# Performance work log

Measured on AMD Instinct MI355X. Metric: run time of the kernel, lower is better.

The kernel has to match this reference:

```python
import jax, jax.numpy as jnp
import numpy as np

N_NODES = 100000
N_EDGES = 1600000
D_IN = 128
D_OUT = 128
NUM_NEIGHBORS = 10


def setup_inputs() -> dict:
    key = jax.random.key(0)
    k1, k2, k3, k4 = jax.random.split(key, 4)
    x = jax.random.normal(k1, (N_NODES, D_IN), dtype=jnp.float32)
    edge_index = jax.random.randint(k2, (2, N_EDGES), 0, N_NODES, dtype=jnp.int64)
    W = jax.random.normal(k3, (D_OUT, D_IN), dtype=jnp.float32) / np.sqrt(D_IN)
    b = jax.random.normal(k4, (D_OUT,), dtype=jnp.float32) * 0.01
    return {"x": x, "edge_index": edge_index, "W": W, "b": b}


def reference(x, edge_index, W, b):
    # Torch semantics: for each node, take the FIRST num_neighbors edges
    # (in original edge order) with row==node, mean their col features;
    # fall back to x[node] if the node has no out-edges. Then linear.
    row, col = edge_index[0], edge_index[1]
    N, E = x.shape[0], row.shape[0]
    # Stable sort by row preserves within-row edge order, so "first k per row"
    # is identical to the torch masking loop.
    order = jnp.argsort(row, stable=True)
    row_s = row[order]
    col_s = col[order]
    # Index of first edge of each row segment -> per-edge rank within segment.
    starts = jnp.searchsorted(row_s, jnp.arange(N, dtype=row_s.dtype))
    rank = jnp.arange(E) - starts[row_s]
    keep = (rank < NUM_NEIGHBORS).astype(x.dtype)  # [E]
    # Masked gather + segment sum == sampled neighbor mean numerator.
    feats = x[col_s] * keep[:, None]               # [E, D_IN] (gather-bound)
    sums = jax.ops.segment_sum(feats, row_s, num_segments=N)
    counts = jax.ops.segment_sum(keep, row_s, num_segments=N)  # [N]
    agg = jnp.where(counts[:, None] > 0,
                    sums / jnp.maximum(counts, 1.0)[:, None],
                    x)
    return agg @ W.T + b
```

## Files before the change

### kernel.cpp

```cpp
#include <hip/hip_runtime.h>
#include <hip/hip_bf16.h>
#include <cstdint>
#include <cstddef>

#define D 128
#define KNB 10
#define SENT 0x7FFFFFFF
#define SHIFT 8
#define NPB 256
#define T_BIN 256
#define EPB 4096
#define MAXNB 1024

typedef __attribute__((ext_vector_type(8))) short short8;
typedef __attribute__((ext_vector_type(4))) float floatx4;

__device__ inline unsigned bf16_rne(float f) {
  unsigned u = __builtin_bit_cast(unsigned, f);
  return (u + 0x7FFFu + ((u >> 16) & 1u)) >> 16;
}
__device__ inline float bflo(unsigned u) { return __builtin_bit_cast(float, u << 16); }
__device__ inline float bfhi(unsigned u) { return __builtin_bit_cast(float, u & 0xFFFF0000u); }

__global__ __launch_bounds__(256) void k_init(int* __restrict__ counts, int NB) {
  int i = blockIdx.x * 256 + threadIdx.x;
  if (i < NB) counts[i] = 0;
}

__global__ __launch_bounds__(T_BIN) void k_count_xcast(const int* __restrict__ row, int E,
                                                       int NB, int* __restrict__ counts,
                                                       int blocks_bin,
                                                       const float* __restrict__ x,
                                                       unsigned* __restrict__ xh, int n8) {
  if ((int)blockIdx.x < blocks_bin) {
    __shared__ int hist[MAXNB];
    for (int i = threadIdx.x; i < NB; i += T_BIN) hist[i] = 0;
    __syncthreads();
    int e0 = blockIdx.x * EPB;
    for (int i = threadIdx.x; i < EPB; i += T_BIN) {
      int e = e0 + i;
      if (e < E) atomicAdd(&hist[row[e] >> SHIFT], 1);
    }
    __syncthreads();
    for (int i = threadIdx.x; i < NB; i += T_BIN)
      if (hist[i]) atomicAdd(&counts[i], hist[i]);
  } else {
    int t = ((int)blockIdx.x - blocks_bin) * T_BIN + threadIdx.x;
    if (t >= n8) return;
    const float4* p = reinterpret_cast<const float4*>(x) + (size_t)t * 2;
    float4 a = p[0], b = p[1];
    uint4 o;
    o.x = bf16_rne(a.x) | (bf16_rne(a.y) << 16);
    o.y = bf16_rne(a.z) | (bf16_rne(a.w) << 16);
    o.z = bf16_rne(b.x) | (bf16_rne(b.y) << 16);
    o.w = bf16_rne(b.z) | (bf16_rne(b.w) << 16);
    reinterpret_cast<uint4*>(xh)[t] = o;
  }
}

__global__ __launch_bounds__(MAXNB) void k_scan(const int* __restrict__ counts, int NB,
                                                int* __restrict__ bases,
                                                int* __restrict__ cursor) {
  __shared__ int buf[MAXNB];
  int t = threadIdx.x;
  int v = (t < NB) ? counts[t] : 0;
  buf[t] = v;
  __syncthreads();
  for (int off = 1; off < MAXNB; off <<= 1) {
    int xv = (t >= off) ? buf[t - off] : 0;
    __syncthreads();
    buf[t] += xv;
    __syncthreads();
  }
  if (t < NB) {
    int base = buf[t] - v;
    bases[t] = base;
    cursor[t] = base;
  }
}

__global__ __launch_bounds__(T_BIN) void k_scatter2(const int* __restrict__ row, int E,
                                                    int NB, int* __restrict__ cursor,
                                                    unsigned* __restrict__ binned) {
  __shared__ int hist[MAXNB];
  __shared__ int lbase[MAXNB];
  for (int i = threadIdx.x; i < NB; i += T_BIN) hist[i] = 0;
  __syncthreads();
  int e0 = blockIdx.x * EPB;
  for (int i = threadIdx.x; i < EPB; i += T_BIN) {
    int e = e0 + i;
    if (e < E) atomicAdd(&hist[row[e] >> SHIFT], 1);
  }
  __syncthreads();
  for (int i = threadIdx.x; i < NB; i += T_BIN) {
    int h = hist[i];
    lbase[i] = h ? atomicAdd(&cursor[i], h) : 0;
  }
  __syncthreads();
  for (int i = threadIdx.x; i < NB; i += T_BIN) hist[i] = 0;
  __syncthreads();
  for (int i = threadIdx.x; i < EPB; i += T_BIN) {
    int e = e0 + i;
    if (e < E) {
      int r = row[e];
      int b = r >> SHIFT;
      int pos = lbase[b] + atomicAdd(&hist[b], 1);
      binned[pos] = ((unsigned)(r & (NPB - 1)) << 24) | (unsigned)e;
    }
  }
}

__global__ __launch_bounds__(256) void k_select(const unsigned* __restrict__ binned,
                                                const int* __restrict__ bases,
                                                const int* __restrict__ counts,
                                                const int* __restrict__ ei,
                                                int* __restrict__ slots_g, int N, int E) {
  __shared__ int sl[NPB * KNB];
  int b = blockIdx.x;
  int nbase = b << SHIFT;
  int nloc = min(NPB, N - nbase);
  for (int i = threadIdx.x; i < nloc * KNB; i += 256) sl[i] = SENT;
  __syncthreads();
  int base = bases[b];
  int cnt = counts[b];
  if (cnt > E) cnt = E;
  for (int i = threadIdx.x; i < cnt; i += 256) {
    unsigned en = binned[base + i];
    int rl = (int)(en >> 24);
    int v = (int)(en & 0xFFFFFFu);
    int* s = &sl[rl * KNB];
#pragma unroll
    for (int k = 0; k < KNB; ++k) {
      int old = atomicMin(&s[k], v);
      if (old == SENT) break;
      v = v > old ? v : old;
    }
  }
  __syncthreads();
  for (int i = threadIdx.x; i < nloc * KNB; i += 256) {
    int v = sl[i];
    int col = ((unsigned)v < (unsigned)E) ? ei[(size_t)E + v] : -1;
    slots_g[(size_t)nbase * KNB + i] = col;
  }
}

__global__ __launch_bounds__(256) void k_agg_hb(const unsigned* __restrict__ xh,
                                                const float* __restrict__ x,
                                                const int* __restrict__ slots,
                                                unsigned* __restrict__ aggbh,
                                                int N) {
  const int lane = threadIdx.x & 63;
  const int j16 = lane & 15;
  const int gsh = lane & 48;
  const int n = blockIdx.x * 16 + (threadIdx.x >> 4);
  const bool active = n < N;

  int scol = -1;
  if (active && j16 < KNB) scol = slots[(size_t)n * KNB + j16];
  bool valid = (unsigned)scol < (unsigned)N;
  unsigned long long bal = __ballot(valid);
  int nsel = __popc((unsigned)((bal >> gsh) & 0xFFFFull));

  int ck[KNB];
#pragma unroll
  for (int k = 0; k < KNB; ++k) ck[k] = __shfl(scol, gsh + k);

  const uint4* xh4 = reinterpret_cast<const uint4*>(xh);
  uint4 uu[KNB];
  float wj[KNB];
#pragma unroll
  for (int k = 0; k < KNB; ++k) {
    bool vk = (unsigned)ck[k] < (unsigned)N;
    wj[k] = vk ? 1.f : 0.f;
    uu[k] = xh4[(size_t)(vk ? ck[k] : 0) * 16 + j16];
  }

  if (!active) return;

  float acc[8];
#pragma unroll
  for (int q = 0; q < 8; ++q) acc[q] = 0.f;

  if (nsel > 0) {
#pragma unroll
    for (int k = 0; k < KNB; ++k) {
      float w = wj[k];
      acc[0] += w * bflo(uu[k].x); acc[1] += w * bfhi(uu[k].x);
      acc[2] += w * bflo(uu[k].y); acc[3] += w * bfhi(uu[k].y);
      acc[4] += w * bflo(uu[k].z); acc[5] += w * bfhi(uu[k].z);
      acc[6] += w * bflo(uu[k].w); acc[7] += w * bfhi(uu[k].w);
    }
    float sc = 1.f / (float)nsel;
#pragma unroll
    for (int q = 0; q < 8; ++q) acc[q] *= sc;
  } else {
    const float4* xr = reinterpret_cast<const float4*>(x + (size_t)n * D);
    float4 v0 = xr[j16 * 2], v1 = xr[j16 * 2 + 1];
    acc[0] = v0.x; acc[1] = v0.y; acc[2] = v0.z; acc[3] = v0.w;
    acc[4] = v1.x; acc[5] = v1.y; acc[6] = v1.z; acc[7] = v1.w;
  }

  uint4 o;
  o.x = bf16_rne(acc[0]) | (bf16_rne(acc[1]) << 16);
  o.y = bf16_rne(acc[2]) | (bf16_rne(acc[3]) << 16);
  o.z = bf16_rne(acc[4]) | (bf16_rne(acc[5]) << 16);
  o.w = bf16_rne(acc[6]) | (bf16_rne(acc[7]) << 16);
  reinterpret_cast<uint4*>(aggbh)[(size_t)n * 16 + j16] = o;
}

__global__ __launch_bounds__(256) void k_agg_h(const unsigned* __restrict__ xh,
                                               const float* __restrict__ x,
                                               const int* __restrict__ slots,
                                               float* __restrict__ agg, int N) {
  int wave = threadIdx.x >> 6;
  int lane = threadIdx.x & 63;
  int n = blockIdx.x * 4 + wave;
  if (n >= N) return;
  int c = -1;
  if (lane < KNB) c = slots[(size_t)n * KNB + lane];
  bool valid = (lane < KNB) && ((unsigned)c < (unsigned)N);
  unsigned long long m = __ballot(valid);
  int nsel = __popcll(m);
  float ax = 0.f, ay = 0.f;
  if (nsel > 0) {
    unsigned long long mm = m;
    while (mm) {
      int j = (int)__builtin_ctzll(mm);
      mm &= mm - 1;
      int cj = __shfl(c, j);
      if ((unsigned)cj >= (unsigned)N) cj = 0;
      unsigned u = xh[(size_t)cj * 64 + lane];
      ax += bflo(u);
      ay += bfhi(u);
    }
    float sc = 1.f / (float)nsel;
    ax *= sc; ay *= sc;
  } else {
    float2 v = reinterpret_cast<const float2*>(x + (size_t)n * D)[lane];
    ax = v.x; ay = v.y;
  }
  reinterpret_cast<float2*>(agg + (size_t)n * D)[lane] = make_float2(ax, ay);
}

__global__ __launch_bounds__(256) void k_agg(const float* __restrict__ x,
                                             const int* __restrict__ slots,
                                             float* __restrict__ agg,
                                             int N) {
  int wave = threadIdx.x >> 6;
  int lane = threadIdx.x & 63;
  int n = blockIdx.x * 4 + wave;
  if (n >= N) return;
  int c = -1;
  if (lane < KNB) c = slots[(size_t)n * KNB + lane];
  bool valid = (lane < KNB) && ((unsigned)c < (unsigned)N);
  unsigned long long m = __ballot(valid);
  int nsel = __popcll(m);
  float2 acc = make_float2(0.f, 0.f);
  if (nsel > 0) {
    unsigned long long mm = m;
    while (mm) {
      int j = (int)__builtin_ctzll(mm);
      mm &= mm - 1;
      int cj = __shfl(c, j);
      if ((unsigned)cj >= (unsigned)N) cj = 0;
      float2 v = reinterpret_cast<const float2*>(x + (size_t)cj * D)[lane];
      acc.x += v.x; acc.y += v.y;
    }
    float sc = 1.f / (float)nsel;
    acc.x *= sc; acc.y *= sc;
  } else {
    acc = reinterpret_cast<const float2*>(x + (size_t)n * D)[lane];
  }
  reinterpret_cast<float2*>(agg + (size_t)n * D)[lane] = acc;
}

#define GBN 128
#define LDK 136

__global__ __launch_bounds__(256) void k_gemm_bf(const unsigned short* __restrict__ aggbh,
                                                 const float* __restrict__ Wm,
                                                 const float* __restrict__ bias,
                                                 float* __restrict__ out, int N) {
  __shared__ unsigned short sA[GBN * LDK];
  __shared__ unsigned short sW[GBN * LDK];
  const int tid = threadIdx.x;
  const int n0 = blockIdx.x * GBN;

#pragma unroll
  for (int i = 0; i < 8; ++i) {
    int q = i * 256 + tid;
    int row = q >> 4;
    int c16 = q & 15;
    uint4 v = make_uint4(0u, 0u, 0u, 0u);
    if (n0 + row < N)
      v = reinterpret_cast<const uint4*>(aggbh + (size_t)(n0 + row) * D)[c16];
    *reinterpret_cast<uint4*>(&sA[row * LDK + c16 * 8]) = v;
  }
#pragma unroll
  for (int i = 0; i < 16; ++i) {
    int q = i * 256 + tid;
    int row = q >> 5;
    int c4 = q & 31;
    float4 wv = reinterpret_cast<const float4*>(Wm + (size_t)row * D)[c4];
    ushort4 uw;
    uw.x = (unsigned short)bf16_rne(wv.x);
    uw.y = (unsigned short)bf16_rne(wv.y);
    uw.z = (unsigned short)bf16_rne(wv.z);
    uw.w = (unsigned short)bf16_rne(wv.w);
    *reinterpret_cast<ushort4*>(&sW[row * LDK + c4 * 4]) = uw;
  }
  __syncthreads();

  const int wave = tid >> 6;
  const int lane = tid & 63;
  const int lrow = lane & 15;
  const int quad = lane >> 4;

  floatx4 acc[2][8];
#pragma unroll
  for (int mt = 0; mt < 2; ++mt)
#pragma unroll
    for (int nt = 0; nt < 8; ++nt)
      acc[mt][nt] = (floatx4){0.f, 0.f, 0.f, 0.f};

  float bv[8];
#pragma unroll
  for (int nt = 0; nt < 8; ++nt) bv[nt] = bias[nt * 16 + lrow];

#pragma unroll
  for (int ks = 0; ks < 4; ++ks) {
    int koff = ks * 32 + quad * 8;
    short8 a0 = *reinterpret_cast<const short8*>(&sA[(wave * 32 + lrow) * LDK + koff]);
    short8 a1 = *reinterpret_cast<const short8*>(&sA[(wave * 32 + 16 + lrow) * LDK + koff]);
#pragma unroll
    for (int nt = 0; nt < 8; ++nt) {
      short8 b = *reinterpret_cast<const short8*>(&sW[(nt * 16 + lrow) * LDK + koff]);
      acc[0][nt] = __builtin_amdgcn_mfma_f32_16x16x32_bf16(a0, b, acc[0][nt], 0, 0, 0);
      acc[1][nt] = __builtin_amdgcn_mfma_f32_16x16x32_bf16(a1, b, acc[1][nt], 0, 0, 0);
    }
  }

#pragma unroll
  for (int mt = 0; mt < 2; ++mt) {
    int rbase = n0 + wave * 32 + mt * 16 + quad * 4;
#pragma unroll
    for (int reg = 0; reg < 4; ++reg) {
      int r = rbase + reg;
      if (r < N) {
        float* op = out + (size_t)r * D + lrow;
#pragma unroll
        for (int nt = 0; nt < 8; ++nt)
          op[nt * 16] = acc[mt][nt][reg] + bv[nt];
      }
    }
  }
}

#define BN 128
#define KC 32
#define LDP 132

__global__ __launch_bounds__(256) void k_gemm(const float* __restrict__ agg,
                                              const float* __restrict__ Wm,
                                              const float* __restrict__ bias,
                                              float* __restrict__ out, int N) {
  __shared__ float sA[KC][LDP];
  __shared__ float sW[KC][LDP];
  const int tid = threadIdx.x;
  const int tx = tid & 15;
  const int ty = tid >> 4;
  const int n0 = blockIdx.x * BN;

  float acc[8][8];
#pragma unroll
  for (int i = 0; i < 8; ++i)
#pragma unroll
    for (int j = 0; j < 8; ++j) acc[i][j] = 0.f;

  const int nl = tid >> 3;
  const int kq = tid & 7;

  for (int kc = 0; kc < D; kc += KC) {
#pragma unroll
    for (int i = 0; i < 4; ++i) {
      int rrow = nl + i * 32;
      int n = n0 + rrow;
      float4 av = make_float4(0.f, 0.f, 0.f, 0.f);
      if (n < N)
        av = reinterpret_cast<const float4*>(agg + (size_t)n * D + kc)[kq];
      int k = kq * 4;
      sA[k+0][rrow] = av.x; sA[k+1][rrow] = av.y;
      sA[k+2][rrow] = av.z; sA[k+3][rrow] = av.w;
      float4 wv = reinterpret_cast<const float4*>(Wm + (size_t)rrow * D + kc)[kq];
      sW[k+0][rrow] = wv.x; sW[k+1][rrow] = wv.y;
      sW[k+2][rrow] = wv.z; sW[k+3][rrow] = wv.w;
    }
    __syncthreads();
#pragma unroll
    for (int k = 0; k < KC; ++k) {
      float4 a0 = *reinterpret_cast<const float4*>(&sA[k][ty * 8]);
      float4 a1 = *reinterpret_cast<const float4*>(&sA[k][ty * 8 + 4]);
      float4 w0 = *reinterpret_cast<const float4*>(&sW[k][tx * 8]);
      float4 w1 = *reinterpret_cast<const float4*>(&sW[k][tx * 8 + 4]);
      float a[8] = {a0.x, a0.y, a0.z, a0.w, a1.x, a1.y, a1.z, a1.w};
      float w[8] = {w0.x, w0.y, w0.z, w0.w, w1.x, w1.y, w1.z, w1.w};
#pragma unroll
      for (int i = 0; i < 8; ++i)
#pragma unroll
        for (int j = 0; j < 8; ++j)
          acc[i][j] += a[i] * w[j];
    }
    __syncthreads();
  }

  float4 b0 = reinterpret_cast<const float4*>(bias)[tx * 2];
  float4 b1 = reinterpret_cast<const float4*>(bias)[tx * 2 + 1];
#pragma unroll
  for (int i = 0; i < 8; ++i) {
    int n = n0 + ty * 8 + i;
    if (n < N) {
      float4 v0 = make_float4(acc[i][0] + b0.x, acc[i][1] + b0.y,
                              acc[i][2] + b0.z, acc[i][3] + b0.w);
      float4 v1 = make_float4(acc[i][4] + b1.x, acc[i][5] + b1.y,
                              acc[i][6] + b1.z, acc[i][7] + b1.w);
      float4* op = reinterpret_cast<float4*>(out + (size_t)n * D + tx * 8);
      op[0] = v0;
      op[1] = v1;
    }
  }
}

extern "C" void kernel_launch(void* const* d_in, const int* in_sizes, int n_in,
                              void* d_out, int out_size, void* d_ws, size_t ws_size,
                              hipStream_t stream) {
  const float* x    = (const float*)d_in[0];
  const int*   ei   = (const int*)d_in[1];
  const float* Wm   = (const float*)d_in[2];
  const float* bias = (const float*)d_in[3];
  float* out = (float*)d_out;

  const int N = in_sizes[0] / D;
  const int E = in_sizes[1] / 2;
  const int NB = (N + NPB - 1) >> SHIFT;

  int* counts = (int*)d_ws;
  int* bases  = counts + NB;
  int* cursor = bases + NB;
  size_t off_slots = ((size_t)(3 * NB) * 4 + 15) & ~(size_t)15;
  int* slots = (int*)((char*)d_ws + off_slots);
  size_t off_xh = (off_slots + (size_t)N * KNB * 4 + 15) & ~(size_t)15;
  unsigned* xh = (unsigned*)((char*)d_ws + off_xh);
  size_t off_ab = off_xh + (size_t)N * D * 2;
  unsigned* aggbh = (unsigned*)((char*)d_ws + off_ab);

  const bool have_xh = ws_size >= off_xh + (size_t)N * D * 2;
  const bool have_ab = ws_size >= off_ab + (size_t)N * D * 2;

  unsigned* binned = (unsigned*)d_out;
  const int blocks_bin = (E + EPB - 1) / EPB;
  const int n8 = N * (D / 8);
  const int xblocks = have_xh ? (n8 + T_BIN - 1) / T_BIN : 0;

  k_init<<<(NB + 255) / 256, 256, 0, stream>>>(counts, NB);
  k_count_xcast<<<blocks_bin + xblocks, T_BIN, 0, stream>>>(ei, E, NB, counts,
                                                            blocks_bin, x, xh, n8);
  k_scan<<<1, MAXNB, 0, stream>>>(counts, NB, bases, cursor);
  k_scatter2<<<blocks_bin, T_BIN, 0, stream>>>(ei, E, NB, cursor, binned);
  k_select<<<NB, 256, 0, stream>>>(binned, bases, counts, ei, slots, N, E);

  if (have_ab) {
    k_agg_hb<<<(N + 15) / 16, 256, 0, stream>>>(xh, x, slots, aggbh, N);
    k_gemm_bf<<<(N + GBN - 1) / GBN, 256, 0, stream>>>(
        (const unsigned short*)aggbh, Wm, bias, out, N);
  } else if (have_xh) {
    k_agg_h<<<(N + 3) / 4, 256, 0, stream>>>(xh, x, slots, out, N);
    k_gemm<<<(N + BN - 1) / BN, 256, 0, stream>>>(out, Wm, bias, out, N);
  } else {
    k_agg<<<(N + 3) / 4, 256, 0, stream>>>(x, slots, out, N);
    k_gemm<<<(N + BN - 1) / BN, 256, 0, stream>>>(out, Wm, bias, out, N);
  }
}
```

Baseline: 232.5 us.

## Fuse neighbor aggregation into bf16 MFMA GEMM kernel via shared memory

Merges the aggregation kernel and the bf16 GEMM into one kernel. Each block gathers and averages 128 nodes' neighbor features straight into LDS as bf16, then runs the MFMA linear layer on them. This removes the global round trip of the aggregated bf16 matrix and one kernel launch. In exchange, a block handles 8 node rows sequentially with a single gather wave pattern, and there are far fewer blocks (782 instead of 6250), which may cut the memory-level parallelism available to hide gather latency. A leftover redundant statement on an unused ushort4 stays in the code.

```diff
diff --git a/kernel.cpp b/kernel.cpp
--- a/kernel.cpp
+++ b/kernel.cpp
@@ -144,102 +144,149 @@
   }
 }
 
-__global__ __launch_bounds__(256) void k_agg_hb(const unsigned* __restrict__ xh,
-                                                const float* __restrict__ x,
-                                                const int* __restrict__ slots,
-                                                unsigned* __restrict__ aggbh,
-                                                int N) {
-  const int lane = threadIdx.x & 63;
+#define GBN 128
+#define LDK 136
+
+__global__ __launch_bounds__(256) void k_fused(const unsigned* __restrict__ xh,
+                                               const float* __restrict__ x,
+                                               const int* __restrict__ slots,
+                                               const float* __restrict__ Wm,
+                                               const float* __restrict__ bias,
+                                               float* __restrict__ out, int N) {
+  __shared__ unsigned short sA[GBN * LDK];
+  __shared__ unsigned short sW[GBN * LDK];
+  const int tid = threadIdx.x;
+  const int n0 = blockIdx.x * GBN;
+
+#pragma unroll
+  for (int i = 0; i < 16; ++i) {
+    int q = i * 256 + tid;
+    int row = q >> 5;
+    int c4 = q & 31;
+    float4 wv = reinterpret_cast<const float4*>(Wm + (size_t)row * D)[c4];
+    ushort4 uw;
+    uw.x = (unsigned short)bf16_rne(wv.x);
+    uw.y = (unsigned short)bf16_rne(wv.y);
+    uw.z = (unsigned short)bf16_rne(wv.z);
+    uw.w = (unsigned short)bf16_rne(wv.w);
+    *reinterpret_cast<ushort4*>(&sW[row * LDK + c4 * 4]) = uw;
+  }
+
+  const int lane = tid & 63;
   const int j16 = lane & 15;
   const int gsh = lane & 48;
-  const int n = blockIdx.x * 16 + (threadIdx.x >> 4);
-  const bool active = n < N;
-
-  int scol = -1;
-  if (active && j16 < KNB) scol = slots[(size_t)n * KNB + j16];
-  bool valid = (unsigned)scol < (unsigned)N;
-  unsigned long long bal = __ballot(valid);
-  int nsel = __popc((unsigned)((bal >> gsh) & 0xFFFFull));
-
-  int ck[KNB];
-#pragma unroll
-  for (int k = 0; k < KNB; ++k) ck[k] = __shfl(scol, gsh + k);
+  const int grp = tid >> 4;
 
   const uint4* xh4 = reinterpret_cast<const uint4*>(xh);
-  uint4 uu[KNB];
-  float wj[KNB];
-#pragma unroll
-  for (int k = 0; k < KNB; ++k) {
-    bool vk = (unsigned)ck[k] < (unsigned)N;
-    wj[k] = vk ? 1.f : 0.f;
-    uu[k] = xh4[(size_t)(vk ? ck[k] : 0) * 16 + j16];
-  }
-
-  if (!active) return;
-
-  float acc[8];
-#pragma unroll
-  for (int q = 0; q < 8; ++q) acc[q] = 0.f;
-
-  if (nsel > 0) {
+
+  for (int nn = 0; nn < 8; ++nn) {
+    const int row = nn * 16 + grp;
+    const int n = n0 + row;
+    const bool active = n < N;
+
+    int scol = -1;
+    if (active && j16 < KNB) scol = slots[(size_t)n * KNB + j16];
+    bool valid = (unsigned)scol < (unsigned)N;
+    unsigned long long bal = __ballot(valid);
+    int nsel = __popc((unsigned)((bal >> gsh) & 0xFFFFull));
+
+    int ck[KNB];
+#pragma unroll
+    for (int k = 0; k < KNB; ++k) ck[k] = __shfl(scol, gsh + k);
+
+    uint4 uu[KNB];
+    float wj[KNB];
 #pragma unroll
     for (int k = 0; k < KNB; ++k) {
-      float w = wj[k];
-      acc[0] += w * bflo(uu[k].x); acc[1] += w * bfhi(uu[k].x);
-      acc[2] += w * bflo(uu[k].y); acc[3] += w * bfhi(uu[k].y);
-      acc[4] += w * bflo(uu[k].z); acc[5] += w * bfhi(uu[k].z);
-      acc[6] += w * bflo(uu[k].w); acc[7] += w * bfhi(uu[k].w);
-    }
-    float sc = 1.f / (float)nsel;
-#pragma unroll
-    for (int q = 0; q < 8; ++q) acc[q] *= sc;
-  } else {
-    const float4* xr = reinterpret_cast<const float4*>(x + (size_t)n * D);
-    float4 v0 = xr[j16 * 2], v1 = xr[j16 * 2 + 1];
-    acc[0] = v0.x; acc[1] = v0.y; acc[2] = v0.z; acc[3] = v0.w;
-    acc[4] = v1.x; acc[5] = v1.y; acc[6] = v1.z; acc[7] = v1.w;
-  }
-
-  uint4 o;
-  o.x = bf16_rne(acc[0]) | (bf16_rne(acc[1]) << 16);
-  o.y = bf16_rne(acc[2]) | (bf16_rne(acc[3]) << 16);
-  o.z = bf16_rne(acc[4]) | (bf16_rne(acc[5]) << 16);
-  o.w = bf16_rne(acc[6]) | (bf16_rne(acc[7]) << 16);
-  reinterpret_cast<uint4*>(aggbh)[(size_t)n * 16 + j16] = o;
-}
-
-__global__ __launch_bounds__(256) void k_agg_h(const unsigned* __restrict__ xh,
-                                               const float* __restrict__ x,
-                                               const int* __restrict__ slots,
-                                               float* __restrict__ agg, int N) {
-  int wave = threadIdx.x >> 6;
-  int lane = threadIdx.x & 63;
-  int n = blockIdx.x * 4 + wave;
-  if (n >= N) return;
-  int c = -1;
-  if (lane < KNB) c = slots[(size_t)n * KNB + lane];
-  bool valid = (lane < KNB) && ((unsigned)c < (unsigned)N);
-  unsigned long long m = __ballot(valid);
-  int nsel = __popcll(m);
-  float ax = 0.f, ay = 0.f;
-  if (nsel > 0) {
-    unsigned long long mm = m;
-    while (mm) {
-      int j = (int)__builtin_ctzll(mm);
-      mm &= mm - 1;
-      int cj = __shfl(c, j);
-      if ((unsigned)cj >= (unsigned)N) cj = 0;
-      unsigned u = xh[(size_t)cj * 64 + lane];
-      ax += bflo(u);
-      ay += bfhi(u);
-    }
-    float sc = 1.f / (float)nsel;
-    ax *= sc; ay *= sc;
-  } else {
-    float2 v = reinterpret_cast<const float2*>(x + (size_t)n * D)[lane];
-    ax = v.x; ay = v.y;
-  }
-  reinterpret_cast<float2*>(agg + (size_t)n * D)[lane] = make_float2(ax, ay);
+      bool vk = (unsigned)ck[k] < (unsigned)N;
+      wj[k] = vk ? 1.f : 0.f;
+      uu[k] = xh4[(size_t)(vk ? ck[k] : 0) * 16 + j16];
+    }
+
+    float acc[8];
+#pragma unroll
+    for (int q = 0; q < 8; ++q) acc[q] = 0.f;
+
+    if (active) {
+      if (nsel > 0) {
+#pragma unroll
+        for (int k = 0; k < KNB; ++k) {
+          float w = wj[k];
+          acc[0] += w * bflo(uu[k].x); acc[1] += w * bfhi(uu[k].x);
+          acc[2] += w * bflo(uu[k].y); acc[3] += w * bfhi(uu[k].y);
+          acc[4] += w * bflo(uu[k].z); acc[5] += w * bfhi(uu[k].z);
+          acc[6] += w * bflo(uu[k].w); acc[7] += w * bfhi(uu[k].w);
+        }
+        float sc = 1.f / (float)nsel;
+#pragma unroll
+        for (int q = 0; q < 8; ++q) acc[q] *= sc;
+      } else {
+        const float4* xr = reinterpret_cast<const float4*>(x + (size_t)n * D);
+        float4 v0 = xr[j16 * 2], v1 = xr[j16 * 2 + 1];
+        acc[0] = v0.x; acc[1] = v0.y; acc[2] = v0.z; acc[3] = v0.w;
+        acc[4] = v1.x; acc[5] = v1.y; acc[6] = v1.z; acc[7] = v1.w;
+      }
+    }
+
+    ushort4 o;
+    o.x = (unsigned short)(bf16_rne(acc[0]) | 0u); o.x = (unsigned short)bf16_rne(acc[0]);
+    ushort4 ow;
+    ow.x = (unsigned short)bf16_rne(acc[0]);
+    ow.y = (unsigned short)bf16_rne(acc[1]);
+    ow.z = (unsigned short)bf16_rne(acc[2]);
+    ow.w = (unsigned short)bf16_rne(acc[3]);
+    ushort4 ow2;
+    ow2.x = (unsigned short)bf16_rne(acc[4]);
+    ow2.y = (unsigned short)bf16_rne(acc[5]);
+    ow2.z = (unsigned short)bf16_rne(acc[6]);
+    ow2.w = (unsigned short)bf16_rne(acc[7]);
+    *reinterpret_cast<ushort4*>(&sA[row * LDK + j16 * 8]) = ow;
+    *reinterpret_cast<ushort4*>(&sA[row * LDK + j16 * 8 + 4]) = ow2;
+  }
+  __syncthreads();
+
+  const int wave = tid >> 6;
+  const int lrow = lane & 15;
+  const int quad = lane >> 4;
+
+  floatx4 acc[2][8];
+#pragma unroll
+  for (int mt = 0; mt < 2; ++mt)
+#pragma unroll
+    for (int nt = 0; nt < 8; ++nt)
+      acc[mt][nt] = (floatx4){0.f, 0.f, 0.f, 0.f};
+
+  float bv[8];
+#pragma unroll
+  for (int nt = 0; nt < 8; ++nt) bv[nt] = bias[nt * 16 + lrow];
+
+#pragma unroll
+  for (int ks = 0; ks < 4; ++ks) {
+    int koff = ks * 32 + quad * 8;
+    short8 a0 = *reinterpret_cast<const short8*>(&sA[(wave * 32 + lrow) * LDK + koff]);
+    short8 a1 = *reinterpret_cast<const short8*>(&sA[(wave * 32 + 16 + lrow) * LDK + koff]);
+#pragma unroll
+    for (int nt = 0; nt < 8; ++nt) {
+      short8 b = *reinterpret_cast<const short8*>(&sW[(nt * 16 + lrow) * LDK + koff]);
+      acc[0][nt] = __builtin_amdgcn_mfma_f32_16x16x32_bf16(a0, b, acc[0][nt], 0, 0, 0);
+      acc[1][nt] = __builtin_amdgcn_mfma_f32_16x16x32_bf16(a1, b, acc[1][nt], 0, 0, 0);
+    }
+  }
+
+#pragma unroll
+  for (int mt = 0; mt < 2; ++mt) {
+    int rbase = n0 + wave * 32 + mt * 16 + quad * 4;
+#pragma unroll
+    for (int reg = 0; reg < 4; ++reg) {
+      int r = rbase + reg;
+      if (r < N) {
+        float* op = out + (size_t)r * D + lrow;
+#pragma unroll
+        for (int nt = 0; nt < 8; ++nt)
+          op[nt * 16] = acc[mt][nt][reg] + bv[nt];
+      }
+    }
+  }
 }
 
 __global__ __launch_bounds__(256) void k_agg(const float* __restrict__ x,
@@ -274,88 +321,6 @@
   reinterpret_cast<float2*>(agg + (size_t)n * D)[lane] = acc;
 }
 
-#define GBN 128
-#define LDK 136
-
-__global__ __launch_bounds__(256) void k_gemm_bf(const unsigned short* __restrict__ aggbh,
-                                                 const float* __restrict__ Wm,
-                                                 const float* __restrict__ bias,
-                                                 float* __restrict__ out, int N) {
-  __shared__ unsigned short sA[GBN * LDK];
-  __shared__ unsigned short sW[GBN * LDK];
-  const int tid = threadIdx.x;
-  const int n0 = blockIdx.x * GBN;
-
-#pragma unroll
-  for (int i = 0; i < 8; ++i) {
-    int q = i * 256 + tid;
-    int row = q >> 4;
-    int c16 = q & 15;
-    uint4 v = make_uint4(0u, 0u, 0u, 0u);
-    if (n0 + row < N)
-      v = reinterpret_cast<const uint4*>(aggbh + (size_t)(n0 + row) * D)[c16];
-    *reinterpret_cast<uint4*>(&sA[row * LDK + c16 * 8]) = v;
-  }
-#pragma unroll
-  for (int i = 0; i < 16; ++i) {
-    int q = i * 256 + tid;
-    int row = q >> 5;
-    int c4 = q & 31;
-    float4 wv = reinterpret_cast<const float4*>(Wm + (size_t)row * D)[c4];
-    ushort4 uw;
-    uw.x = (unsigned short)bf16_rne(wv.x);
-    uw.y = (unsigned short)bf16_rne(wv.y);
-    uw.z = (unsigned short)bf16_rne(wv.z);
-    uw.w = (unsigned short)bf16_rne(wv.w);
-    *reinterpret_cast<ushort4*>(&sW[row * LDK + c4 * 4]) = uw;
-  }
-  __syncthreads();
-
-  const int wave = tid >> 6;
-  const int lane = tid & 63;
-  const int lrow = lane & 15;
-  const int quad = lane >> 4;
-
-  floatx4 acc[2][8];
-#pragma unroll
-  for (int mt = 0; mt < 2; ++mt)
-#pragma unroll
-    for (int nt = 0; nt < 8; ++nt)
-      acc[mt][nt] = (floatx4){0.f, 0.f, 0.f, 0.f};
-
-  float bv[8];
-#pragma unroll
-  for (int nt = 0; nt < 8; ++nt) bv[nt] = bias[nt * 16 + lrow];
-
-#pragma unroll
-  for (int ks = 0; ks < 4; ++ks) {
-    int koff = ks * 32 + quad * 8;
-    short8 a0 = *reinterpret_cast<const short8*>(&sA[(wave * 32 + lrow) * LDK + koff]);
-    short8 a1 = *reinterpret_cast<const short8*>(&sA[(wave * 32 + 16 + lrow) * LDK + koff]);
-#pragma unroll
-    for (int nt = 0; nt < 8; ++nt) {
-      short8 b = *reinterpret_cast<const short8*>(&sW[(nt * 16 + lrow) * LDK + koff]);
-      acc[0][nt] = __builtin_amdgcn_mfma_f32_16x16x32_bf16(a0, b, acc[0][nt], 0, 0, 0);
-      acc[1][nt] = __builtin_amdgcn_mfma_f32_16x16x32_bf16(a1, b, acc[1][nt], 0, 0, 0);
-    }
-  }
-
-#pragma unroll
-  for (int mt = 0; mt < 2; ++mt) {
-    int rbase = n0 + wave * 32 + mt * 16 + quad * 4;
-#pragma unroll
-    for (int reg = 0; reg < 4; ++reg) {
-      int r = rbase + reg;
-      if (r < N) {
-        float* op = out + (size_t)r * D + lrow;
-#pragma unroll
-        for (int nt = 0; nt < 8; ++nt)
-          op[nt * 16] = acc[mt][nt][reg] + bv[nt];
-      }
-    }
-  }
-}
-
 #define BN 128
 #define KC 32
 #define LDP 132
@@ -450,11 +415,8 @@
   int* slots = (int*)((char*)d_ws + off_slots);
   size_t off_xh = (off_slots + (size_t)N * KNB * 4 + 15) & ~(size_t)15;
   unsigned* xh = (unsigned*)((char*)d_ws + off_xh);
-  size_t off_ab = off_xh + (size_t)N * D * 2;
-  unsigned* aggbh = (unsigned*)((char*)d_ws + off_ab);
 
   const bool have_xh = ws_size >= off_xh + (size_t)N * D * 2;
-  const bool have_ab = ws_size >= off_ab + (size_t)N * D * 2;
 
   unsigned* binned = (unsigned*)d_out;
   const int blocks_bin = (E + EPB - 1) / EPB;
@@ -468,13 +430,8 @@
   k_scatter2<<<blocks_bin, T_BIN, 0, stream>>>(ei, E, NB, cursor, binned);
   k_select<<<NB, 256, 0, stream>>>(binned, bases, counts, ei, slots, N, E);
 
-  if (have_ab) {
-    k_agg_hb<<<(N + 15) / 16, 256, 0, stream>>>(xh, x, slots, aggbh, N);
-    k_gemm_bf<<<(N + GBN - 1) / GBN, 256, 0, stream>>>(
-        (const unsigned short*)aggbh, Wm, bias, out, N);
-  } else if (have_xh) {
-    k_agg_h<<<(N + 3) / 4, 256, 0, stream>>>(xh, x, slots, out, N);
-    k_gemm<<<(N + BN - 1) / BN, 256, 0, stream>>>(out, Wm, bias, out, N);
+  if (have_xh) {
+    k_fused<<<(N + GBN - 1) / GBN, 256, 0, stream>>>(xh, x, slots, Wm, bias, out, N);
   } else {
     k_agg<<<(N + 3) / 4, 256, 0, stream>>>(x, slots, out, N);
     k_gemm<<<(N + BN - 1) / BN, 256, 0, stream>>>(out, Wm, bias, out, N);
```

Measured after the change: 224.1 us. -3.6%, faster.
